# Performance work log

Hardware: AMD Instinct MI355X
Metric: run time of the kernel (lower is better)

## Reference

```python
import jax, jax.numpy as jnp
import numpy as np


def ste_sign(x):
    # Forward: q(x) = +1 if x >= 0 else -1.
    # Backward: clipped straight-through estimator (identity on |x| <= 1).
    clipped = jnp.clip(x, -1.0, 1.0)
    binary = jnp.where(x >= 0, 1.0, -1.0).astype(x.dtype)
    return clipped + jax.lax.stop_gradient(binary - clipped)


BATCH = 16384
IN_FEATURES = 4096
UNITS = 512


def setup_inputs() -> dict:
    key = jax.random.key(0)
    kx, kw = jax.random.split(key)
    x = jax.random.normal(kx, (BATCH, IN_FEATURES), dtype=jnp.float32)
    # Latent full-precision kernel (kept in [-1,1]-ish range like a constrained BNN kernel)
    W = jax.random.normal(kw, (IN_FEATURES, UNITS), dtype=jnp.float32) * 0.5
    b = jnp.zeros((UNITS,), dtype=jnp.float32)
    return {"x": x, "W": W, "b": b}


def reference(x, W, b):
    # QuantizedDense: binarize inputs and kernel to +/-1, then standard dense matmul.
    xq = ste_sign(x)                # [B, F]
    Wq = ste_sign(W)                # [F, U]
    return jnp.dot(xq, Wq) + b      # [B, U]
```

## Files before the change

### kernel.cpp

```cpp
#include <hip/hip_runtime.h>
#include <stdint.h>


#define BATCH  16384
#define UNITS  512
#define KDIM   4096
#define KSTEP  64
#define NSTEP  (KDIM / KSTEP)
#define MROWS  32

typedef int v4i  __attribute__((ext_vector_type(4)));
typedef int v16i __attribute__((ext_vector_type(16)));

__global__ __launch_bounds__(256) void pack_w_kernel(const float* __restrict__ W,
                                                     uint8_t* __restrict__ Wb2) {
    int t  = blockIdx.x * 256 + threadIdx.x;
    int n  = t & 511;
    int k0 = (t >> 9) * 8;
    unsigned long long m = 0;
    #pragma unroll
    for (int j = 0; j < 8; ++j) {
        float v = W[(size_t)(k0 + j) * UNITS + n];
        m |= ((v < 0.f) ? 0xFFull : 0x01ull) << (8 * j);
    }
    int s  = k0 >> 6;
    int kk = k0 & 63;
    int ks = kk >> 5;
    int hi = (kk & 31) >> 4;
    int lane = (n & 31) + 32 * hi;
    size_t a = ((((size_t)s * 16 + (n >> 5)) * 2 + ks) * 64 + lane) * 16 + (kk & 15);
    *reinterpret_cast<unsigned long long*>(Wb2 + a) = m;
}

__device__ __forceinline__ uint32_t sgn4(float4 v) {
    uint32_t b0 = v.x < 0.f ? 0xFFu : 0x01u;
    uint32_t b1 = v.y < 0.f ? 0xFFu : 0x01u;
    uint32_t b2 = v.z < 0.f ? 0xFFu : 0x01u;
    uint32_t b3 = v.w < 0.f ? 0xFFu : 0x01u;
    return b0 | (b1 << 8) | (b2 << 16) | (b3 << 24);
}

#define MMSTEP(S, PBUF, XLD, XCM, BLD, BCN)                                    \
    {                                                                          \
        const int cs1 = ((S) + 1 < NSTEP) ? (S) + 1 : NSTEP - 1;               \
        const int cs2 = ((S) + 2 < NSTEP) ? (S) + 2 : NSTEP - 1;               \
        XLD = *reinterpret_cast<const float4*>(xrow + (size_t)cs2 * KSTEP);    \
        const uint8_t* bsrc = bbase + (size_t)cs1 * 32768;                     \
        BLD[0] = *reinterpret_cast<const v4i*>(bsrc);                          \
        BLD[1] = *reinterpret_cast<const v4i*>(bsrc + 1024);                   \
        BLD[2] = *reinterpret_cast<const v4i*>(bsrc + 2048);                   \
        BLD[3] = *reinterpret_cast<const v4i*>(bsrc + 3072);                   \
        v4i af0 = *reinterpret_cast<const v4i*>(&Af[PBUF][0][l * 16]);         \
        v4i af1 = *reinterpret_cast<const v4i*>(&Af[PBUF][1][l * 16]);         \
        __builtin_amdgcn_s_setprio(1);                                         \
        acc0 = __builtin_amdgcn_mfma_i32_32x32x32_i8(af0, BCN[0], acc0, 0, 0, 0); \
        acc0 = __builtin_amdgcn_mfma_i32_32x32x32_i8(af1, BCN[1], acc0, 0, 0, 0); \
        acc1 = __builtin_amdgcn_mfma_i32_32x32x32_i8(af0, BCN[2], acc1, 0, 0, 0); \
        acc1 = __builtin_amdgcn_mfma_i32_32x32x32_i8(af1, BCN[3], acc1, 0, 0, 0); \
        __builtin_amdgcn_s_setprio(0);                                         \
        *reinterpret_cast<uint32_t*>(awp[(PBUF) ^ 1]) = sgn4(XCM);             \
        __syncthreads();                                                       \
    }

__global__ __launch_bounds__(512, 1) void mm_kernel(const float* __restrict__ x,
                                                    const uint8_t* __restrict__ Wb2,
                                                    const float* __restrict__ bias,
                                                    float* __restrict__ C) {
    __shared__ __attribute__((aligned(16))) uint8_t Af[2][2][64 * 16];
    const int t   = threadIdx.x;
    const int l   = t & 63;
    const int wv  = t >> 6;
    const int lr  = l & 31;
    const int hi  = l >> 5;
    const int row0 = blockIdx.x * MROWS;
    const int ar = t >> 4;
    const int ak = (t & 15) * 4;
    const int a_lane = (ar & 31) + 32 * ((ak >> 4) & 1);
    const int a_ks   = ak >> 5;
    const int a_off  = ak & 15;
    uint8_t* awp[2] = { &Af[0][a_ks][a_lane * 16 + a_off],
                        &Af[1][a_ks][a_lane * 16 + a_off] };
    const float* xrow = x + (size_t)(row0 + ar) * KDIM + ak;
    const uint8_t* bbase = Wb2 + ((size_t)(wv * 2) * 2 * 64 + l) * 16;

    v16i acc0, acc1;
    #pragma unroll
    for (int e = 0; e < 16; ++e) { acc0[e] = 0; acc1[e] = 0; }

    float4 xp0, xp1;
    v4i bp0[4], bp1[4];

    {
        float4 x0 = *reinterpret_cast<const float4*>(xrow);
        xp1 = *reinterpret_cast<const float4*>(xrow + KSTEP);
        bp1[0] = *reinterpret_cast<const v4i*>(bbase);
        bp1[1] = *reinterpret_cast<const v4i*>(bbase + 1024);
        bp1[2] = *reinterpret_cast<const v4i*>(bbase + 2048);
        bp1[3] = *reinterpret_cast<const v4i*>(bbase + 3072);
        *reinterpret_cast<uint32_t*>(awp[0]) = sgn4(x0);
        __syncthreads();
    }

    #pragma unroll 1
    for (int s = 0; s < NSTEP; s += 2) {
        MMSTEP(s,     0, xp0, xp1, bp0, bp1);
        MMSTEP(s + 1, 1, xp1, xp0, bp1, bp0);
    }

    #pragma unroll
    for (int ct = 0; ct < 2; ++ct) {
        const int col = wv * 64 + ct * 32 + lr;
        const float bv = bias[col];
        const v16i& a = ct ? acc1 : acc0;
        #pragma unroll
        for (int r = 0; r < 16; ++r) {
            int row = row0 + (r & 3) + 8 * (r >> 2) + 4 * hi;
            C[(size_t)row * UNITS + col] = (float)a[r] + bv;
        }
    }
}

extern "C" void kernel_launch(void* const* d_in, const int* in_sizes, int n_in,
                              void* d_out, int out_size, void* d_ws, size_t ws_size,
                              hipStream_t stream) {
    const float* x = (const float*)d_in[0];
    const float* W = (const float*)d_in[1];
    const float* b = (const float*)d_in[2];
    float* out = (float*)d_out;

    uint8_t* Wb2 = (uint8_t*)d_ws;

    pack_w_kernel<<<(512 * 512) / 256, 256, 0, stream>>>(W, Wb2);
    mm_kernel<<<BATCH / MROWS, 512, 0, stream>>>(x, Wb2, b, out);
}
```

Before: 98.43 us.

## Stage four K-steps of binarized A per barrier to cut syncthreads frequency

The main loop now handles four 64-wide K steps per period. The binarized x tile for all four steps is written into a larger double-buffered shared array, so a block barrier is needed once per four steps instead of every step. B fragments stay register double-buffered and are prefetched one step ahead, while x loads are issued a whole period early. This trades more shared memory and more live registers for fewer barriers and a longer latency window for the x loads.

```diff
diff --git a/kernel.cpp b/kernel.cpp
--- a/kernel.cpp
+++ b/kernel.cpp
@@ -7,6 +7,7 @@
 #define KDIM   4096
 #define KSTEP  64
 #define NSTEP  (KDIM / KSTEP)
+#define NPER   (NSTEP / 4)
 #define MROWS  32
 
 typedef int v4i  __attribute__((ext_vector_type(4)));
@@ -40,25 +41,51 @@
     return b0 | (b1 << 8) | (b2 << 16) | (b3 << 24);
 }
 
-#define MMSTEP(S, PBUF, XLD, XCM, BLD, BCN)                                    \
+#define LOADB(D0, D1, D2, D3, S)                                               \
     {                                                                          \
-        const int cs1 = ((S) + 1 < NSTEP) ? (S) + 1 : NSTEP - 1;               \
-        const int cs2 = ((S) + 2 < NSTEP) ? (S) + 2 : NSTEP - 1;               \
-        XLD = *reinterpret_cast<const float4*>(xrow + (size_t)cs2 * KSTEP);    \
-        const uint8_t* bsrc = bbase + (size_t)cs1 * 32768;                     \
-        BLD[0] = *reinterpret_cast<const v4i*>(bsrc);                          \
-        BLD[1] = *reinterpret_cast<const v4i*>(bsrc + 1024);                   \
-        BLD[2] = *reinterpret_cast<const v4i*>(bsrc + 2048);                   \
-        BLD[3] = *reinterpret_cast<const v4i*>(bsrc + 3072);                   \
-        v4i af0 = *reinterpret_cast<const v4i*>(&Af[PBUF][0][l * 16]);         \
-        v4i af1 = *reinterpret_cast<const v4i*>(&Af[PBUF][1][l * 16]);         \
+        const uint8_t* _b = bbase + (size_t)(S) * 32768;                       \
+        D0 = *reinterpret_cast<const v4i*>(_b);                                \
+        D1 = *reinterpret_cast<const v4i*>(_b + 1024);                         \
+        D2 = *reinterpret_cast<const v4i*>(_b + 2048);                         \
+        D3 = *reinterpret_cast<const v4i*>(_b + 3072);                         \
+    }
+
+#define CLUSTER(PB, FI0, FI1, B0, B1, B2, B3)                                  \
+    {                                                                          \
+        v4i af0 = *reinterpret_cast<const v4i*>(&Af[(PB) * 8192 + (FI0) * 1024 + l * 16]); \
+        v4i af1 = *reinterpret_cast<const v4i*>(&Af[(PB) * 8192 + (FI1) * 1024 + l * 16]); \
         __builtin_amdgcn_s_setprio(1);                                         \
-        acc0 = __builtin_amdgcn_mfma_i32_32x32x32_i8(af0, BCN[0], acc0, 0, 0, 0); \
-        acc0 = __builtin_amdgcn_mfma_i32_32x32x32_i8(af1, BCN[1], acc0, 0, 0, 0); \
-        acc1 = __builtin_amdgcn_mfma_i32_32x32x32_i8(af0, BCN[2], acc1, 0, 0, 0); \
-        acc1 = __builtin_amdgcn_mfma_i32_32x32x32_i8(af1, BCN[3], acc1, 0, 0, 0); \
+        acc0 = __builtin_amdgcn_mfma_i32_32x32x32_i8(af0, B0, acc0, 0, 0, 0);  \
+        acc0 = __builtin_amdgcn_mfma_i32_32x32x32_i8(af1, B1, acc0, 0, 0, 0);  \
+        acc1 = __builtin_amdgcn_mfma_i32_32x32x32_i8(af0, B2, acc1, 0, 0, 0);  \
+        acc1 = __builtin_amdgcn_mfma_i32_32x32x32_i8(af1, B3, acc1, 0, 0, 0);  \
         __builtin_amdgcn_s_setprio(0);                                         \
-        *reinterpret_cast<uint32_t*>(awp[(PBUF) ^ 1]) = sgn4(XCM);             \
+    }
+
+#define PERIOD(Q, PB)                                                          \
+    {                                                                          \
+        const int _s4 = 4 * (Q) + 4;                                           \
+        float4 xq0 = *reinterpret_cast<const float4*>(                         \
+            xrow + (size_t)((_s4     < NSTEP) ? _s4     : NSTEP - 1) * KSTEP); \
+        float4 xq1 = *reinterpret_cast<const float4*>(                         \
+            xrow + (size_t)((_s4 + 1 < NSTEP) ? _s4 + 1 : NSTEP - 1) * KSTEP); \
+        float4 xq2 = *reinterpret_cast<const float4*>(                         \
+            xrow + (size_t)((_s4 + 2 < NSTEP) ? _s4 + 2 : NSTEP - 1) * KSTEP); \
+        float4 xq3 = *reinterpret_cast<const float4*>(                         \
+            xrow + (size_t)((_s4 + 3 < NSTEP) ? _s4 + 3 : NSTEP - 1) * KSTEP); \
+        LOADB(bp1a, bp1b, bp1c, bp1d, 4 * (Q) + 1);                            \
+        CLUSTER(PB, 0, 1, bp0a, bp0b, bp0c, bp0d);                             \
+        LOADB(bp0a, bp0b, bp0c, bp0d, 4 * (Q) + 2);                            \
+        CLUSTER(PB, 2, 3, bp1a, bp1b, bp1c, bp1d);                             \
+        LOADB(bp1a, bp1b, bp1c, bp1d, 4 * (Q) + 3);                            \
+        CLUSTER(PB, 4, 5, bp0a, bp0b, bp0c, bp0d);                             \
+        LOADB(bp0a, bp0b, bp0c, bp0d, (_s4 < NSTEP) ? _s4 : NSTEP - 1);        \
+        CLUSTER(PB, 6, 7, bp1a, bp1b, bp1c, bp1d);                             \
+        uint8_t* _aw = afw + ((PB) ^ 1) * 8192;                                \
+        *reinterpret_cast<uint32_t*>(_aw)        = sgn4(xq0);                  \
+        *reinterpret_cast<uint32_t*>(_aw + 2048) = sgn4(xq1);                  \
+        *reinterpret_cast<uint32_t*>(_aw + 4096) = sgn4(xq2);                  \
+        *reinterpret_cast<uint32_t*>(_aw + 6144) = sgn4(xq3);                  \
         __syncthreads();                                                       \
     }
 
@@ -66,7 +93,7 @@
                                                     const uint8_t* __restrict__ Wb2,
                                                     const float* __restrict__ bias,
                                                     float* __restrict__ C) {
-    __shared__ __attribute__((aligned(16))) uint8_t Af[2][2][64 * 16];
+    __shared__ __attribute__((aligned(16))) uint8_t Af[2 * 8 * 1024];
     const int t   = threadIdx.x;
     const int l   = t & 63;
     const int wv  = t >> 6;
@@ -78,8 +105,7 @@
     const int a_lane = (ar & 31) + 32 * ((ak >> 4) & 1);
     const int a_ks   = ak >> 5;
     const int a_off  = ak & 15;
-    uint8_t* awp[2] = { &Af[0][a_ks][a_lane * 16 + a_off],
-                        &Af[1][a_ks][a_lane * 16 + a_off] };
+    uint8_t* afw = &Af[a_ks * 1024 + a_lane * 16 + a_off];
     const float* xrow = x + (size_t)(row0 + ar) * KDIM + ak;
     const uint8_t* bbase = Wb2 + ((size_t)(wv * 2) * 2 * 64 + l) * 16;
 
@@ -87,24 +113,25 @@
     #pragma unroll
     for (int e = 0; e < 16; ++e) { acc0[e] = 0; acc1[e] = 0; }
 
-    float4 xp0, xp1;
-    v4i bp0[4], bp1[4];
+    v4i bp0a, bp0b, bp0c, bp0d, bp1a, bp1b, bp1c, bp1d;
 
     {
         float4 x0 = *reinterpret_cast<const float4*>(xrow);
-        xp1 = *reinterpret_cast<const float4*>(xrow + KSTEP);
-        bp1[0] = *reinterpret_cast<const v4i*>(bbase);
-        bp1[1] = *reinterpret_cast<const v4i*>(bbase + 1024);
-        bp1[2] = *reinterpret_cast<const v4i*>(bbase + 2048);
-        bp1[3] = *reinterpret_cast<const v4i*>(bbase + 3072);
-        *reinterpret_cast<uint32_t*>(awp[0]) = sgn4(x0);
+        float4 x1 = *reinterpret_cast<const float4*>(xrow + KSTEP);
+        float4 x2 = *reinterpret_cast<const float4*>(xrow + 2 * KSTEP);
+        float4 x3 = *reinterpret_cast<const float4*>(xrow + 3 * KSTEP);
+        LOADB(bp0a, bp0b, bp0c, bp0d, 0);
+        *reinterpret_cast<uint32_t*>(afw)        = sgn4(x0);
+        *reinterpret_cast<uint32_t*>(afw + 2048) = sgn4(x1);
+        *reinterpret_cast<uint32_t*>(afw + 4096) = sgn4(x2);
+        *reinterpret_cast<uint32_t*>(afw + 6144) = sgn4(x3);
         __syncthreads();
     }
 
     #pragma unroll 1
-    for (int s = 0; s < NSTEP; s += 2) {
-        MMSTEP(s,     0, xp0, xp1, bp0, bp1);
-        MMSTEP(s + 1, 1, xp1, xp0, bp1, bp0);
+    for (int q = 0; q < NPER; q += 2) {
+        PERIOD(q,     0);
+        PERIOD(q + 1, 1);
     }
 
     #pragma unroll
```

Result: faster. 94.91 us (-3.6%).
